# Optimization experiments

Hardware: AMD Instinct MI355X
Metric: run time of the kernel (lower is better)

The kernel has to match this reference:

```python
import jax, jax.numpy as jnp
import numpy as np

N_NODES = 100000


def gcn_conv(x, W, b, src, dst, n):
    """PyG GCNConv: add self-loops, symmetric degree norm, linear, scatter-add."""
    loop = jnp.arange(n, dtype=src.dtype)
    s = jnp.concatenate([src, loop])  # source nodes (message origin)
    d = jnp.concatenate([dst, loop])  # target nodes (aggregation)
    deg = jax.ops.segment_sum(jnp.ones_like(d, dtype=x.dtype), d, num_segments=n)
    dinv = jnp.where(deg > 0, jax.lax.rsqrt(deg), 0.0)
    norm = dinv[s] * dinv[d]  # [E+N]
    h = x @ W  # [N, out]
    msg = h[s] * norm[:, None]  # [E+N, out]
    return jax.ops.segment_sum(msg, d, num_segments=n) + b


def setup_inputs() -> dict:
    key = jax.random.key(0)
    ks = jax.random.split(key, 8)
    n, e, din, dh, dout = N_NODES, 3200000, 128, 64, 6
    x = jax.random.normal(ks[0], (n, din), dtype=jnp.float32)
    edge_index = jax.random.randint(ks[1], (2, e), 0, n, dtype=jnp.int64)
    sc = lambda f: 1.0 / np.sqrt(f)
    W1 = jax.random.normal(ks[2], (din, dh), dtype=jnp.float32) * sc(din)
    b1 = jnp.zeros((dh,), dtype=jnp.float32)
    W2 = jax.random.normal(ks[3], (dh, dh), dtype=jnp.float32) * sc(dh)
    b2 = jnp.zeros((dh,), dtype=jnp.float32)
    W3 = jax.random.normal(ks[4], (dh, dout), dtype=jnp.float32) * sc(dh)
    b3 = jnp.zeros((dout,), dtype=jnp.float32)
    return {"x": x, "edge_index": edge_index, "W1": W1, "b1": b1,
            "W2": W2, "b2": b2, "W3": W3, "b3": b3}


def reference(x, edge_index, W1, b1, W2, b2, W3, b3):
    n = x.shape[0]
    src, dst = edge_index[0], edge_index[1]
    # eval mode: dropout is identity
    h = jax.nn.relu(gcn_conv(x, W1, b1, src, dst, n))
    h = jax.nn.relu(gcn_conv(h, W2, b2, src, dst, n))
    h = gcn_conv(h, W3, b3, src, dst, n)
    return jax.nn.log_softmax(h, axis=1)
```

## Files before the change

kernel.cpp:

```cpp
#include <hip/hip_runtime.h>
#include <hip/hip_fp16.h>
#include <math.h>


#define WS_ALIGN(x) (((x) + 255) & ~(size_t)255)
#define BKN 256
#define CAP 9216
#define EPT 8
#define BIN_THR 512
#define BIN_CHUNK (BIN_THR * EPT)

typedef _Float16 half8 __attribute__((ext_vector_type(8)));
typedef float floatx4 __attribute__((ext_vector_type(4)));

__global__ __launch_bounds__(BIN_THR) void bin_kernel(
    const int* __restrict__ src, const int* __restrict__ dst,
    int* __restrict__ cur, int* __restrict__ slab, int E, int NB) {
    __shared__ int cnt[512];
    __shared__ int incl[512];
    __shared__ int gbase[512];
    __shared__ int stag[BIN_CHUNK];
    const int tid = threadIdx.x;
    const int base = blockIdx.x * BIN_CHUNK + tid * EPT;
    cnt[tid] = 0;
    __syncthreads();
    int b[EPT], w[EPT], lp[EPT];
    #pragma unroll
    for (int k = 0; k < EPT; ++k) {
        int e = base + k;
        if (e < E) {
            int s = src[e], d = dst[e];
            b[k] = d >> 8;
            w[k] = (s << 8) | (d & 255);
        } else b[k] = -1;
    }
    #pragma unroll
    for (int k = 0; k < EPT; ++k)
        if (b[k] >= 0) lp[k] = atomicAdd(&cnt[b[k]], 1);
    __syncthreads();
    incl[tid] = cnt[tid];
    __syncthreads();
    for (int off = 1; off < 512; off <<= 1) {
        int v = 0;
        if (tid >= off) v = incl[tid - off];
        __syncthreads();
        incl[tid] += v;
        __syncthreads();
    }
    if (tid < NB) {
        int c = cnt[tid];
        gbase[tid] = c ? atomicAdd(&cur[tid], c) : 0;
    }
    #pragma unroll
    for (int k = 0; k < EPT; ++k)
        if (b[k] >= 0) stag[incl[b[k]] - cnt[b[k]] + lp[k]] = w[k];
    __syncthreads();
    const int total = incl[NB - 1];
    for (int idx = tid; idx < total; idx += BIN_THR) {
        int wv = stag[idx];
        int lo = 0, hi = NB - 1;
        while (lo < hi) { int mid = (lo + hi) >> 1; if (incl[mid] > idx) hi = mid; else lo = mid + 1; }
        int excl = incl[lo] - cnt[lo];
        int p = gbase[lo] + (idx - excl);
        if (p < CAP) slab[(size_t)lo * CAP + p] = wv;
    }
}

__global__ __launch_bounds__(512) void bucket_sort_kernel(
    const int* __restrict__ slab, const int* __restrict__ cur,
    int* __restrict__ srcS, int2* __restrict__ rows,
    float* __restrict__ dinv, int n) {
    __shared__ int cnt[BKN], s[BKN], cursor[BKN];
    const int b = blockIdx.x, tid = threadIdx.x;
    const int m = min(cur[b], CAP);
    const int* sp = slab + (size_t)b * CAP;
    if (tid < BKN) cnt[tid] = 0;
    __syncthreads();
    for (int j = tid; j < m; j += 512) atomicAdd(&cnt[sp[j] & (BKN - 1)], 1);
    __syncthreads();
    if (tid < BKN) s[tid] = cnt[tid];
    __syncthreads();
    for (int off = 1; off < BKN; off <<= 1) {
        int v = 0;
        if (tid < BKN && tid >= off) v = s[tid - off];
        __syncthreads();
        if (tid < BKN) s[tid] += v;
        __syncthreads();
    }
    if (tid < BKN) {
        int ofs = s[tid] - cnt[tid];
        cursor[tid] = ofs;
        int node = b * BKN + tid;
        if (node < n) {
            rows[node] = make_int2(b * CAP + ofs, b * CAP + ofs + cnt[tid]);
            dinv[node] = rsqrtf((float)(cnt[tid] + 1));
        }
    }
    __syncthreads();
    for (int j = tid; j < m; j += 512) {
        int w = sp[j];
        int p = atomicAdd(&cursor[w & (BKN - 1)], 1);
        srcS[(size_t)b * CAP + p] = w >> 8;
    }
}

template <int K>
__global__ __launch_bounds__(256) void linear_mfma_f32_kernel(
    const float* __restrict__ Xf, const float* __restrict__ W,
    const float* __restrict__ dinv, _Float16* __restrict__ Y, int n) {
    constexpr int KC = K / 32;
    __shared__ _Float16 Bf[KC * 4 * 64 * 8];
    const int tid = threadIdx.x;
    for (int i = tid; i < KC * 4 * 64 * 8; i += 256) {
        int j = i & 7, lane = (i >> 3) & 63, tile = (i >> 9) & 3, kc = i >> 11;
        int k = kc * 32 + ((lane >> 4) << 3) + j;
        int col = tile * 16 + (lane & 15);
        Bf[i] = (_Float16)W[k * 64 + col];
    }
    __syncthreads();
    const int lane = tid & 63, wid = tid >> 6;
    const int mrow = lane & 15, quad = lane >> 4;
    #pragma unroll
    for (int tt = 0; tt < 4; ++tt) {
        const int base = (blockIdx.x * 4 + tt) * 64 + wid * 16;
        if (base >= n) continue;
        const int anode = min(base + mrow, n - 1);
        floatx4 acc[4] = {{0, 0, 0, 0}, {0, 0, 0, 0}, {0, 0, 0, 0}, {0, 0, 0, 0}};
        #pragma unroll
        for (int kc = 0; kc < KC; ++kc) {
            float4 xa = *(const float4*)&Xf[(size_t)anode * K + kc * 32 + quad * 8];
            float4 xb = *(const float4*)&Xf[(size_t)anode * K + kc * 32 + quad * 8 + 4];
            half8 a;
            a[0] = (_Float16)xa.x; a[1] = (_Float16)xa.y; a[2] = (_Float16)xa.z; a[3] = (_Float16)xa.w;
            a[4] = (_Float16)xb.x; a[5] = (_Float16)xb.y; a[6] = (_Float16)xb.z; a[7] = (_Float16)xb.w;
            #pragma unroll
            for (int t = 0; t < 4; ++t) {
                half8 b = *(const half8*)&Bf[((kc * 4 + t) * 64 + lane) * 8];
                acc[t] = __builtin_amdgcn_mfma_f32_16x16x32_f16(a, b, acc[t], 0, 0, 0);
            }
        }
        #pragma unroll
        for (int r = 0; r < 4; ++r) {
            int node = base + quad * 4 + r;
            if (node < n) {
                float di = dinv[node];
                #pragma unroll
                for (int t = 0; t < 4; ++t)
                    Y[(size_t)node * 64 + t * 16 + mrow] = (_Float16)(acc[t][r] * di);
            }
        }
    }
}

__global__ __launch_bounds__(256) void linear_mfma_f16_kernel(
    const _Float16* __restrict__ Xh, const float* __restrict__ W,
    const float* __restrict__ dinv, _Float16* __restrict__ Y, int n) {
    constexpr int K = 64, KC = 2;
    __shared__ _Float16 Bf[KC * 4 * 64 * 8];
    const int tid = threadIdx.x;
    for (int i = tid; i < KC * 4 * 64 * 8; i += 256) {
        int j = i & 7, lane = (i >> 3) & 63, tile = (i >> 9) & 3, kc = i >> 11;
        int k = kc * 32 + ((lane >> 4) << 3) + j;
        int col = tile * 16 + (lane & 15);
        Bf[i] = (_Float16)W[k * 64 + col];
    }
    __syncthreads();
    const int lane = tid & 63, wid = tid >> 6;
    const int mrow = lane & 15, quad = lane >> 4;
    #pragma unroll
    for (int tt = 0; tt < 4; ++tt) {
        const int base = (blockIdx.x * 4 + tt) * 64 + wid * 16;
        if (base >= n) continue;
        const int anode = min(base + mrow, n - 1);
        floatx4 acc[4] = {{0, 0, 0, 0}, {0, 0, 0, 0}, {0, 0, 0, 0}, {0, 0, 0, 0}};
        #pragma unroll
        for (int kc = 0; kc < KC; ++kc) {
            half8 a = *(const half8*)&Xh[(size_t)anode * K + kc * 32 + quad * 8];
            #pragma unroll
            for (int t = 0; t < 4; ++t) {
                half8 b = *(const half8*)&Bf[((kc * 4 + t) * 64 + lane) * 8];
                acc[t] = __builtin_amdgcn_mfma_f32_16x16x32_f16(a, b, acc[t], 0, 0, 0);
            }
        }
        #pragma unroll
        for (int r = 0; r < 4; ++r) {
            int node = base + quad * 4 + r;
            if (node < n) {
                float di = dinv[node];
                #pragma unroll
                for (int t = 0; t < 4; ++t)
                    Y[(size_t)node * 64 + t * 16 + mrow] = (_Float16)(acc[t][r] * di);
            }
        }
    }
}

__global__ __launch_bounds__(256) void linear3_kernel(const __half* __restrict__ Xh,
                                                      const float* __restrict__ W,
                                                      const float* __restrict__ dinv,
                                                      __half* __restrict__ Y, int n) {
    __shared__ float Wl[64 * 6];
    __shared__ float Xs[32][65];
    const int tid = threadIdx.x;
    for (int i = tid; i < 64 * 6; i += 256) Wl[i] = W[i];
    const int sub = tid >> 3;
    const int feat = tid & 7;
    for (int base = blockIdx.x * 32; base < n; base += gridDim.x * 32) {
        __syncthreads();
        for (int i = tid; i < 32 * 64; i += 256) {
            int r = i >> 6, c = i & 63;
            int node = base + r;
            Xs[r][c] = (node < n) ? __half2float(Xh[(size_t)node * 64 + c]) : 0.f;
        }
        __syncthreads();
        int node = base + sub;
        if (node < n) {
            float r = 0.f;
            if (feat < 6) {
                float acc = 0.f;
                #pragma unroll
                for (int k = 0; k < 64; ++k) acc = fmaf(Xs[sub][k], Wl[k * 6 + feat], acc);
                r = acc * dinv[node];
            }
            Y[(size_t)node * 8 + feat] = __float2half_rn(r);
        }
    }
}

__global__ __launch_bounds__(256) void agg64_kernel(
    const _Float16* __restrict__ Hs, const float* __restrict__ dinv,
    const int* __restrict__ srcS, const int2* __restrict__ rows,
    const float* __restrict__ bias, _Float16* __restrict__ Out,
    int n, int do_relu) {
    const int wave = (blockIdx.x * blockDim.x + threadIdx.x) >> 6;
    const int lane = threadIdx.x & 63;
    if (wave >= n) return;
    const int slot = lane >> 3;
    const int f8 = lane & 7;
    const int2 row = rows[wave];
    const int beg = row.x, end = row.y;
    half8 hA, hB;
    #pragma unroll
    for (int i = 0; i < 8; ++i) { hA[i] = (_Float16)0.f; hB[i] = (_Float16)0.f; }
    int j = beg;
    for (; j + 32 <= end; j += 32) {
        int s0 = srcS[j      + slot];
        int s1 = srcS[j + 8  + slot];
        int s2 = srcS[j + 16 + slot];
        int s3 = srcS[j + 24 + slot];
        half8 v0 = *(const half8*)&Hs[(size_t)s0 * 64 + f8 * 8];
        half8 v1 = *(const half8*)&Hs[(size_t)s1 * 64 + f8 * 8];
        half8 v2 = *(const half8*)&Hs[(size_t)s2 * 64 + f8 * 8];
        half8 v3 = *(const half8*)&Hs[(size_t)s3 * 64 + f8 * 8];
        hA += v0; hB += v1; hA += v2; hB += v3;
    }
    for (; j + 16 <= end; j += 16) {
        int s0 = srcS[j + slot];
        int s1 = srcS[j + 8 + slot];
        half8 v0 = *(const half8*)&Hs[(size_t)s0 * 64 + f8 * 8];
        half8 v1 = *(const half8*)&Hs[(size_t)s1 * 64 + f8 * 8];
        hA += v0; hB += v1;
    }
    for (; j < end; j += 8) {
        int jj = j + slot;
        if (jj < end) {
            half8 v = *(const half8*)&Hs[(size_t)srcS[jj] * 64 + f8 * 8];
            hA += v;
        }
    }
    half8 ht = hA + hB;
    #pragma unroll
    for (int mask = 8; mask <= 32; mask <<= 1) {
        int4 ci = *(int4*)&ht, oi;
        oi.x = __shfl_xor(ci.x, mask);
        oi.y = __shfl_xor(ci.y, mask);
        oi.z = __shfl_xor(ci.z, mask);
        oi.w = __shfl_xor(ci.w, mask);
        ht += *(half8*)&oi;
    }
    half8 self = *(const half8*)&Hs[(size_t)wave * 64 + f8 * 8];
    const float di = dinv[wave];
    float4 b0 = *(const float4*)&bias[f8 * 8];
    float4 b1 = *(const float4*)&bias[f8 * 8 + 4];
    float bb[8] = {b0.x, b0.y, b0.z, b0.w, b1.x, b1.y, b1.z, b1.w};
    half8 o;
    #pragma unroll
    for (int i = 0; i < 8; ++i) {
        float t = ((float)ht[i] + (float)self[i]) * di + bb[i];
        if (do_relu) t = fmaxf(t, 0.f);
        o[i] = (_Float16)t;
    }
    if (slot == 0) *(half8*)&Out[(size_t)wave * 64 + f8 * 8] = o;
}

__global__ __launch_bounds__(256) void agg6_lsm_kernel(
    const _Float16* __restrict__ Hs6, const float* __restrict__ dinv,
    const int* __restrict__ srcS, const int2* __restrict__ rows,
    const float* __restrict__ bias, float* __restrict__ out, int n) {
    const int wave = (blockIdx.x * blockDim.x + threadIdx.x) >> 6;
    const int lane = threadIdx.x & 63;
    if (wave >= n) return;
    const int2 row = rows[wave];
    const int beg = row.x, end = row.y;
    half8 ht;
    #pragma unroll
    for (int i = 0; i < 8; ++i) ht[i] = (_Float16)0.f;
    for (int j = beg + lane; j < end; j += 64) {
        int s = srcS[j];
        ht += *(const half8*)&Hs6[(size_t)s * 8];
    }
    #pragma unroll
    for (int mask = 1; mask <= 32; mask <<= 1) {
        int4 ci = *(int4*)&ht, oi;
        oi.x = __shfl_xor(ci.x, mask);
        oi.y = __shfl_xor(ci.y, mask);
        oi.z = __shfl_xor(ci.z, mask);
        oi.w = __shfl_xor(ci.w, mask);
        ht += *(half8*)&oi;
    }
    half8 self = *(const half8*)&Hs6[(size_t)wave * 8];
    const float di = dinv[wave];
    float a[6];
    #pragma unroll
    for (int q = 0; q < 6; ++q)
        a[q] = ((float)ht[q] + (float)self[q]) * di + bias[q];
    float mx = a[0];
    #pragma unroll
    for (int q = 1; q < 6; ++q) mx = fmaxf(mx, a[q]);
    float sum = 0.f;
    #pragma unroll
    for (int q = 0; q < 6; ++q) sum += expf(a[q] - mx);
    float lse = mx + logf(sum);
    if (lane == 0) {
        float* op = &out[(size_t)wave * 6];
        *(float2*)(op)     = make_float2(a[0] - lse, a[1] - lse);
        *(float2*)(op + 2) = make_float2(a[2] - lse, a[3] - lse);
        *(float2*)(op + 4) = make_float2(a[4] - lse, a[5] - lse);
    }
}

extern "C" void kernel_launch(void* const* d_in, const int* in_sizes, int n_in,
                              void* d_out, int out_size, void* d_ws, size_t ws_size,
                              hipStream_t stream) {
    const float* x  = (const float*)d_in[0];
    const int*   ei = (const int*)d_in[1];
    const float* W1 = (const float*)d_in[2];
    const float* b1 = (const float*)d_in[3];
    const float* W2 = (const float*)d_in[4];
    const float* b2 = (const float*)d_in[5];
    const float* W3 = (const float*)d_in[6];
    const float* b3 = (const float*)d_in[7];
    float* out = (float*)d_out;

    const int n = in_sizes[0] / 128;
    const int E = in_sizes[1] / 2;
    const int* src = ei;
    const int* dst = ei + E;
    const int NB = (n + BKN - 1) / BKN;

    char* ws = (char*)d_ws;
    auto carve = [&](size_t bytes) { char* p = ws; ws += WS_ALIGN(bytes); return p; };
    int*      cur  = (int*)     carve((size_t)NB * 4);
    float*    dinv = (float*)   carve((size_t)n * 4);
    int*      slab = (int*)     carve((size_t)NB * CAP * 4);
    int*      srcS = (int*)     carve((size_t)NB * CAP * 4);
    int2*     rows = (int2*)    carve((size_t)n * 8);
    _Float16* hsA  = (_Float16*)carve((size_t)n * 64 * 2 + 4096);
    _Float16* hsB  = (_Float16*)carve((size_t)n * 64 * 2 + 4096);
    _Float16* hsC  = (_Float16*)carve((size_t)n * 8 * 2);
    (void)ws_size; (void)n_in; (void)out_size;

    (void)hipMemsetAsync(cur, 0, (size_t)NB * 4, stream);
    bin_kernel<<<(E + BIN_CHUNK - 1) / BIN_CHUNK, BIN_THR, 0, stream>>>(src, dst, cur, slab, E, NB);
    bucket_sort_kernel<<<NB, 512, 0, stream>>>(slab, cur, srcS, rows, dinv, n);

    const int aggGrid = (n + 3) / 4;
    const int linGrid = (n + 255) / 256;

    linear_mfma_f32_kernel<128><<<linGrid, 256, 0, stream>>>(x, W1, dinv, hsA, n);
    agg64_kernel<<<aggGrid, 256, 0, stream>>>(hsA, dinv, srcS, rows, b1, hsB, n, 1);

    linear_mfma_f16_kernel<<<linGrid, 256, 0, stream>>>(hsB, W2, dinv, hsA, n);
    agg64_kernel<<<aggGrid, 256, 0, stream>>>(hsA, dinv, srcS, rows, b2, hsB, n, 1);

    linear3_kernel<<<2048, 256, 0, stream>>>((const __half*)hsB, W3, dinv, (__half*)hsC, n);
    agg6_lsm_kernel<<<(n + 3) / 4, 256, 0, stream>>>(hsC, dinv, srcS, rows, b3, out, n);
}
```

Measured before the change: 356.0 us.

## Aggregate before transform in layer 2 and fuse layer-2/3 linears into aggregation

```diff
diff --git a/kernel.cpp b/kernel.cpp
--- a/kernel.cpp
+++ b/kernel.cpp
@@ -11,6 +11,7 @@
 #define BIN_CHUNK (BIN_THR * EPT)
 
 typedef _Float16 half8 __attribute__((ext_vector_type(8)));
+typedef _Float16 half2v __attribute__((ext_vector_type(2)));
 typedef float floatx4 __attribute__((ext_vector_type(4)));
 
 __global__ __launch_bounds__(BIN_THR) void bin_kernel(
@@ -121,8 +122,8 @@
     const int lane = tid & 63, wid = tid >> 6;
     const int mrow = lane & 15, quad = lane >> 4;
     #pragma unroll
-    for (int tt = 0; tt < 4; ++tt) {
-        const int base = (blockIdx.x * 4 + tt) * 64 + wid * 16;
+    for (int tt = 0; tt < 2; ++tt) {
+        const int base = (blockIdx.x * 2 + tt) * 64 + wid * 16;
         if (base >= n) continue;
         const int anode = min(base + mrow, n - 1);
         floatx4 acc[4] = {{0, 0, 0, 0}, {0, 0, 0, 0}, {0, 0, 0, 0}, {0, 0, 0, 0}};
@@ -152,86 +153,11 @@
     }
 }
 
-__global__ __launch_bounds__(256) void linear_mfma_f16_kernel(
-    const _Float16* __restrict__ Xh, const float* __restrict__ W,
-    const float* __restrict__ dinv, _Float16* __restrict__ Y, int n) {
-    constexpr int K = 64, KC = 2;
-    __shared__ _Float16 Bf[KC * 4 * 64 * 8];
-    const int tid = threadIdx.x;
-    for (int i = tid; i < KC * 4 * 64 * 8; i += 256) {
-        int j = i & 7, lane = (i >> 3) & 63, tile = (i >> 9) & 3, kc = i >> 11;
-        int k = kc * 32 + ((lane >> 4) << 3) + j;
-        int col = tile * 16 + (lane & 15);
-        Bf[i] = (_Float16)W[k * 64 + col];
-    }
-    __syncthreads();
-    const int lane = tid & 63, wid = tid >> 6;
-    const int mrow = lane & 15, quad = lane >> 4;
-    #pragma unroll
-    for (int tt = 0; tt < 4; ++tt) {
-        const int base = (blockIdx.x * 4 + tt) * 64 + wid * 16;
-        if (base >= n) continue;
-        const int anode = min(base + mrow, n - 1);
-        floatx4 acc[4] = {{0, 0, 0, 0}, {0, 0, 0, 0}, {0, 0, 0, 0}, {0, 0, 0, 0}};
-        #pragma unroll
-        for (int kc = 0; kc < KC; ++kc) {
-            half8 a = *(const half8*)&Xh[(size_t)anode * K + kc * 32 + quad * 8];
-            #pragma unroll
-            for (int t = 0; t < 4; ++t) {
-                half8 b = *(const half8*)&Bf[((kc * 4 + t) * 64 + lane) * 8];
-                acc[t] = __builtin_amdgcn_mfma_f32_16x16x32_f16(a, b, acc[t], 0, 0, 0);
-            }
-        }
-        #pragma unroll
-        for (int r = 0; r < 4; ++r) {
-            int node = base + quad * 4 + r;
-            if (node < n) {
-                float di = dinv[node];
-                #pragma unroll
-                for (int t = 0; t < 4; ++t)
-                    Y[(size_t)node * 64 + t * 16 + mrow] = (_Float16)(acc[t][r] * di);
-            }
-        }
-    }
-}
-
-__global__ __launch_bounds__(256) void linear3_kernel(const __half* __restrict__ Xh,
-                                                      const float* __restrict__ W,
-                                                      const float* __restrict__ dinv,
-                                                      __half* __restrict__ Y, int n) {
-    __shared__ float Wl[64 * 6];
-    __shared__ float Xs[32][65];
-    const int tid = threadIdx.x;
-    for (int i = tid; i < 64 * 6; i += 256) Wl[i] = W[i];
-    const int sub = tid >> 3;
-    const int feat = tid & 7;
-    for (int base = blockIdx.x * 32; base < n; base += gridDim.x * 32) {
-        __syncthreads();
-        for (int i = tid; i < 32 * 64; i += 256) {
-            int r = i >> 6, c = i & 63;
-            int node = base + r;
-            Xs[r][c] = (node < n) ? __half2float(Xh[(size_t)node * 64 + c]) : 0.f;
-        }
-        __syncthreads();
-        int node = base + sub;
-        if (node < n) {
-            float r = 0.f;
-            if (feat < 6) {
-                float acc = 0.f;
-                #pragma unroll
-                for (int k = 0; k < 64; ++k) acc = fmaf(Xs[sub][k], Wl[k * 6 + feat], acc);
-                r = acc * dinv[node];
-            }
-            Y[(size_t)node * 8 + feat] = __float2half_rn(r);
-        }
-    }
-}
-
 __global__ __launch_bounds__(256) void agg64_kernel(
     const _Float16* __restrict__ Hs, const float* __restrict__ dinv,
     const int* __restrict__ srcS, const int2* __restrict__ rows,
     const float* __restrict__ bias, _Float16* __restrict__ Out,
-    int n, int do_relu) {
+    int n, int do_relu, int post_scale) {
     const int wave = (blockIdx.x * blockDim.x + threadIdx.x) >> 6;
     const int lane = threadIdx.x & 63;
     if (wave >= n) return;
@@ -288,9 +214,115 @@
     for (int i = 0; i < 8; ++i) {
         float t = ((float)ht[i] + (float)self[i]) * di + bb[i];
         if (do_relu) t = fmaxf(t, 0.f);
+        if (post_scale) t *= di;
         o[i] = (_Float16)t;
     }
     if (slot == 0) *(half8*)&Out[(size_t)wave * 64 + f8 * 8] = o;
+}
+
+__global__ __launch_bounds__(256) void aggB_kernel(
+    const _Float16* __restrict__ H1s, const float* __restrict__ dinv,
+    const int* __restrict__ srcS, const int2* __restrict__ rows,
+    const float* __restrict__ W2, const float* __restrict__ b2,
+    const float* __restrict__ W3, __half* __restrict__ Yc, int n) {
+    __shared__ half2v W2p[32 * 64];
+    __shared__ float  W3l[64 * 6];
+    __shared__ _Float16 uL[4][64];
+    const int tid = threadIdx.x;
+    for (int i = tid; i < 32 * 64; i += 256) {
+        int t = i >> 6, o = i & 63;
+        half2v v;
+        v[0] = (_Float16)W2[(2 * t) * 64 + o];
+        v[1] = (_Float16)W2[(2 * t + 1) * 64 + o];
+        W2p[i] = v;
+    }
+    for (int i = tid; i < 64 * 6; i += 256) W3l[i] = W3[i];
+    __syncthreads();
+    const int wid = tid >> 6, lane = tid & 63;
+    const int wave = blockIdx.x * 4 + wid;
+    if (wave >= n) return;
+    const int slot = lane >> 3;
+    const int f8 = lane & 7;
+    const int2 row = rows[wave];
+    const int beg = row.x, end = row.y;
+    half8 hA, hB;
+    #pragma unroll
+    for (int i = 0; i < 8; ++i) { hA[i] = (_Float16)0.f; hB[i] = (_Float16)0.f; }
+    int j = beg;
+    for (; j + 32 <= end; j += 32) {
+        int s0 = srcS[j      + slot];
+        int s1 = srcS[j + 8  + slot];
+        int s2 = srcS[j + 16 + slot];
+        int s3 = srcS[j + 24 + slot];
+        half8 v0 = *(const half8*)&H1s[(size_t)s0 * 64 + f8 * 8];
+        half8 v1 = *(const half8*)&H1s[(size_t)s1 * 64 + f8 * 8];
+        half8 v2 = *(const half8*)&H1s[(size_t)s2 * 64 + f8 * 8];
+        half8 v3 = *(const half8*)&H1s[(size_t)s3 * 64 + f8 * 8];
+        hA += v0; hB += v1; hA += v2; hB += v3;
+    }
+    for (; j + 16 <= end; j += 16) {
+        int s0 = srcS[j + slot];
+        int s1 = srcS[j + 8 + slot];
+        half8 v0 = *(const half8*)&H1s[(size_t)s0 * 64 + f8 * 8];
+        half8 v1 = *(const half8*)&H1s[(size_t)s1 * 64 + f8 * 8];
+        hA += v0; hB += v1;
+    }
+    for (; j < end; j += 8) {
+        int jj = j + slot;
+        if (jj < end) {
+            half8 v = *(const half8*)&H1s[(size_t)srcS[jj] * 64 + f8 * 8];
+            hA += v;
+        }
+    }
+    half8 ht = hA + hB;
+    #pragma unroll
+    for (int mask = 8; mask <= 32; mask <<= 1) {
+        int4 ci = *(int4*)&ht, oi;
+        oi.x = __shfl_xor(ci.x, mask);
+        oi.y = __shfl_xor(ci.y, mask);
+        oi.z = __shfl_xor(ci.z, mask);
+        oi.w = __shfl_xor(ci.w, mask);
+        ht += *(half8*)&oi;
+    }
+    half8 self = *(const half8*)&H1s[(size_t)wave * 64 + f8 * 8];
+    const float di = dinv[wave];
+    half8 u;
+    #pragma unroll
+    for (int i = 0; i < 8; ++i)
+        u[i] = (_Float16)(((float)ht[i] + (float)self[i]) * di);
+    if (slot == 0) *(half8*)&uL[wid][f8 * 8] = u;
+    float acc = b2[lane];
+    const half2v* up = (const half2v*)&uL[wid][0];
+    #pragma unroll
+    for (int t = 0; t < 32; ++t) {
+        half2v uv = up[t];
+        half2v wv = W2p[t * 64 + lane];
+#if defined(__has_builtin)
+#if __has_builtin(__builtin_amdgcn_fdot2)
+        acc = __builtin_amdgcn_fdot2(uv, wv, acc, false);
+#else
+        acc += (float)uv[0] * (float)wv[0] + (float)uv[1] * (float)wv[1];
+#endif
+#else
+        acc += (float)uv[0] * (float)wv[0] + (float)uv[1] * (float)wv[1];
+#endif
+    }
+    float h2 = fmaxf(acc, 0.f);
+    float p[6];
+    #pragma unroll
+    for (int q = 0; q < 6; ++q) p[q] = h2 * W3l[lane * 6 + q];
+    #pragma unroll
+    for (int mask = 1; mask <= 32; mask <<= 1) {
+        #pragma unroll
+        for (int q = 0; q < 6; ++q) p[q] += __shfl_xor(p[q], mask);
+    }
+    if (lane == 0) {
+        half8 o;
+        #pragma unroll
+        for (int q = 0; q < 6; ++q) o[q] = (_Float16)(p[q] * di);
+        o[6] = (_Float16)0.f; o[7] = (_Float16)0.f;
+        *(half8*)&Yc[(size_t)wave * 8] = o;
+    }
 }
 
 __global__ __launch_bounds__(256) void agg6_lsm_kernel(
@@ -375,14 +407,12 @@
     bucket_sort_kernel<<<NB, 512, 0, stream>>>(slab, cur, srcS, rows, dinv, n);
 
     const int aggGrid = (n + 3) / 4;
-    const int linGrid = (n + 255) / 256;
+    const int linGrid = (n + 127) / 128;
 
     linear_mfma_f32_kernel<128><<<linGrid, 256, 0, stream>>>(x, W1, dinv, hsA, n);
-    agg64_kernel<<<aggGrid, 256, 0, stream>>>(hsA, dinv, srcS, rows, b1, hsB, n, 1);
-
-    linear_mfma_f16_kernel<<<linGrid, 256, 0, stream>>>(hsB, W2, dinv, hsA, n);
-    agg64_kernel<<<aggGrid, 256, 0, stream>>>(hsA, dinv, srcS, rows, b2, hsB, n, 1);
-
-    linear3_kernel<<<2048, 256, 0, stream>>>((const __half*)hsB, W3, dinv, (__half*)hsC, n);
-    agg6_lsm_kernel<<<(n + 3) / 4, 256, 0, stream>>>(hsC, dinv, srcS, rows, b3, out, n);
-}
+    agg64_kernel<<<aggGrid, 256, 0, stream>>>(hsA, dinv, srcS, rows, b1, hsB, n, 1, 1);
+
+    aggB_kernel<<<aggGrid, 256, 0, stream>>>(hsB, dinv, srcS, rows, W2, b2, W3, (__half*)hsC, n);
+
+    agg6_lsm_kernel<<<aggGrid, 256, 0, stream>>>(hsC, dinv, srcS, rows, b3, out, n);
+}
```

Result: slower. 379.6 us (+6.6%).

## Fuse edge binning with layer-1 linear and fold layer-3 linear into aggregation

Applied to the files above, without the earlier changes.

```diff
diff --git a/kernel.cpp b/kernel.cpp
--- a/kernel.cpp
+++ b/kernel.cpp
@@ -13,56 +13,103 @@
 typedef _Float16 half8 __attribute__((ext_vector_type(8)));
 typedef float floatx4 __attribute__((ext_vector_type(4)));
 
-__global__ __launch_bounds__(BIN_THR) void bin_kernel(
+__global__ __launch_bounds__(512) void fat_bin_lin1_kernel(
     const int* __restrict__ src, const int* __restrict__ dst,
-    int* __restrict__ cur, int* __restrict__ slab, int E, int NB) {
-    __shared__ int cnt[512];
-    __shared__ int incl[512];
-    __shared__ int gbase[512];
-    __shared__ int stag[BIN_CHUNK];
+    int* __restrict__ cur, int* __restrict__ slab, int E, int NB, int binG,
+    const float* __restrict__ Xf, const float* __restrict__ W1,
+    _Float16* __restrict__ Y, int n) {
+    __shared__ int smem[5632];
     const int tid = threadIdx.x;
-    const int base = blockIdx.x * BIN_CHUNK + tid * EPT;
-    cnt[tid] = 0;
-    __syncthreads();
-    int b[EPT], w[EPT], lp[EPT];
-    #pragma unroll
-    for (int k = 0; k < EPT; ++k) {
-        int e = base + k;
-        if (e < E) {
-            int s = src[e], d = dst[e];
-            b[k] = d >> 8;
-            w[k] = (s << 8) | (d & 255);
-        } else b[k] = -1;
-    }
-    #pragma unroll
-    for (int k = 0; k < EPT; ++k)
-        if (b[k] >= 0) lp[k] = atomicAdd(&cnt[b[k]], 1);
-    __syncthreads();
-    incl[tid] = cnt[tid];
-    __syncthreads();
-    for (int off = 1; off < 512; off <<= 1) {
-        int v = 0;
-        if (tid >= off) v = incl[tid - off];
-        __syncthreads();
-        incl[tid] += v;
-        __syncthreads();
-    }
-    if (tid < NB) {
-        int c = cnt[tid];
-        gbase[tid] = c ? atomicAdd(&cur[tid], c) : 0;
-    }
-    #pragma unroll
-    for (int k = 0; k < EPT; ++k)
-        if (b[k] >= 0) stag[incl[b[k]] - cnt[b[k]] + lp[k]] = w[k];
-    __syncthreads();
-    const int total = incl[NB - 1];
-    for (int idx = tid; idx < total; idx += BIN_THR) {
-        int wv = stag[idx];
-        int lo = 0, hi = NB - 1;
-        while (lo < hi) { int mid = (lo + hi) >> 1; if (incl[mid] > idx) hi = mid; else lo = mid + 1; }
-        int excl = incl[lo] - cnt[lo];
-        int p = gbase[lo] + (idx - excl);
-        if (p < CAP) slab[(size_t)lo * CAP + p] = wv;
+    if (blockIdx.x < binG) {
+        int* cnt   = smem;
+        int* incl  = smem + 512;
+        int* gbase = smem + 1024;
+        int* stag  = smem + 1536;
+        const int base = blockIdx.x * BIN_CHUNK + tid * EPT;
+        cnt[tid] = 0;
+        __syncthreads();
+        int b[EPT], w[EPT], lp[EPT];
+        #pragma unroll
+        for (int k = 0; k < EPT; ++k) {
+            int e = base + k;
+            if (e < E) {
+                int s = src[e], d = dst[e];
+                b[k] = d >> 8;
+                w[k] = (s << 8) | (d & 255);
+            } else b[k] = -1;
+        }
+        #pragma unroll
+        for (int k = 0; k < EPT; ++k)
+            if (b[k] >= 0) lp[k] = atomicAdd(&cnt[b[k]], 1);
+        __syncthreads();
+        incl[tid] = cnt[tid];
+        __syncthreads();
+        for (int off = 1; off < 512; off <<= 1) {
+            int v = 0;
+            if (tid >= off) v = incl[tid - off];
+            __syncthreads();
+            incl[tid] += v;
+            __syncthreads();
+        }
+        if (tid < NB) {
+            int c = cnt[tid];
+            gbase[tid] = c ? atomicAdd(&cur[tid], c) : 0;
+        }
+        #pragma unroll
+        for (int k = 0; k < EPT; ++k)
+            if (b[k] >= 0) stag[incl[b[k]] - cnt[b[k]] + lp[k]] = w[k];
+        __syncthreads();
+        const int total = incl[NB - 1];
+        for (int idx = tid; idx < total; idx += BIN_THR) {
+            int wv = stag[idx];
+            int lo = 0, hi = NB - 1;
+            while (lo < hi) { int mid = (lo + hi) >> 1; if (incl[mid] > idx) hi = mid; else lo = mid + 1; }
+            int excl = incl[lo] - cnt[lo];
+            int p = gbase[lo] + (idx - excl);
+            if (p < CAP) slab[(size_t)lo * CAP + p] = wv;
+        }
+    } else {
+        constexpr int K = 128, KC = 4;
+        _Float16* Bf = (_Float16*)smem;
+        for (int i = tid; i < KC * 4 * 64 * 8; i += 512) {
+            int j = i & 7, lane = (i >> 3) & 63, tile = (i >> 9) & 3, kc = i >> 11;
+            int k = kc * 32 + ((lane >> 4) << 3) + j;
+            int col = tile * 16 + (lane & 15);
+            Bf[i] = (_Float16)W1[k * 64 + col];
+        }
+        __syncthreads();
+        const int lane = tid & 63, wid = tid >> 6;
+        const int mrow = lane & 15, quad = lane >> 4;
+        const int lblk = blockIdx.x - binG;
+        #pragma unroll
+        for (int tt = 0; tt < 2; ++tt) {
+            const int base = lblk * 256 + wid * 32 + tt * 16;
+            if (base >= n) continue;
+            const int anode = min(base + mrow, n - 1);
+            floatx4 acc[4] = {{0, 0, 0, 0}, {0, 0, 0, 0}, {0, 0, 0, 0}, {0, 0, 0, 0}};
+            #pragma unroll
+            for (int kc = 0; kc < KC; ++kc) {
+                float4 xa = *(const float4*)&Xf[(size_t)anode * K + kc * 32 + quad * 8];
+                float4 xb = *(const float4*)&Xf[(size_t)anode * K + kc * 32 + quad * 8 + 4];
+                half8 a;
+                a[0] = (_Float16)xa.x; a[1] = (_Float16)xa.y; a[2] = (_Float16)xa.z; a[3] = (_Float16)xa.w;
+                a[4] = (_Float16)xb.x; a[5] = (_Float16)xb.y; a[6] = (_Float16)xb.z; a[7] = (_Float16)xb.w;
+                #pragma unroll
+                for (int t = 0; t < 4; ++t) {
+                    half8 b = *(const half8*)&Bf[((kc * 4 + t) * 64 + lane) * 8];
+                    acc[t] = __builtin_amdgcn_mfma_f32_16x16x32_f16(a, b, acc[t], 0, 0, 0);
+                }
+            }
+            #pragma unroll
+            for (int r = 0; r < 4; ++r) {
+                int node = base + quad * 4 + r;
+                if (node < n) {
+                    #pragma unroll
+                    for (int t = 0; t < 4; ++t)
+                        Y[(size_t)node * 64 + t * 16 + mrow] = (_Float16)acc[t][r];
+                }
+            }
+        }
     }
 }
 
@@ -101,54 +148,6 @@
         int w = sp[j];
         int p = atomicAdd(&cursor[w & (BKN - 1)], 1);
         srcS[(size_t)b * CAP + p] = w >> 8;
-    }
-}
-
-template <int K>
-__global__ __launch_bounds__(256) void linear_mfma_f32_kernel(
-    const float* __restrict__ Xf, const float* __restrict__ W,
-    const float* __restrict__ dinv, _Float16* __restrict__ Y, int n) {
-    constexpr int KC = K / 32;
-    __shared__ _Float16 Bf[KC * 4 * 64 * 8];
-    const int tid = threadIdx.x;
-    for (int i = tid; i < KC * 4 * 64 * 8; i += 256) {
-        int j = i & 7, lane = (i >> 3) & 63, tile = (i >> 9) & 3, kc = i >> 11;
-        int k = kc * 32 + ((lane >> 4) << 3) + j;
-        int col = tile * 16 + (lane & 15);
-        Bf[i] = (_Float16)W[k * 64 + col];
-    }
-    __syncthreads();
-    const int lane = tid & 63, wid = tid >> 6;
-    const int mrow = lane & 15, quad = lane >> 4;
-    #pragma unroll
-    for (int tt = 0; tt < 4; ++tt) {
-        const int base = (blockIdx.x * 4 + tt) * 64 + wid * 16;
-        if (base >= n) continue;
-        const int anode = min(base + mrow, n - 1);
-        floatx4 acc[4] = {{0, 0, 0, 0}, {0, 0, 0, 0}, {0, 0, 0, 0}, {0, 0, 0, 0}};
-        #pragma unroll
-        for (int kc = 0; kc < KC; ++kc) {
-            float4 xa = *(const float4*)&Xf[(size_t)anode * K + kc * 32 + quad * 8];
-            float4 xb = *(const float4*)&Xf[(size_t)anode * K + kc * 32 + quad * 8 + 4];
-            half8 a;
-            a[0] = (_Float16)xa.x; a[1] = (_Float16)xa.y; a[2] = (_Float16)xa.z; a[3] = (_Float16)xa.w;
-            a[4] = (_Float16)xb.x; a[5] = (_Float16)xb.y; a[6] = (_Float16)xb.z; a[7] = (_Float16)xb.w;
-            #pragma unroll
-            for (int t = 0; t < 4; ++t) {
-                half8 b = *(const half8*)&Bf[((kc * 4 + t) * 64 + lane) * 8];
-                acc[t] = __builtin_amdgcn_mfma_f32_16x16x32_f16(a, b, acc[t], 0, 0, 0);
-            }
-        }
-        #pragma unroll
-        for (int r = 0; r < 4; ++r) {
-            int node = base + quad * 4 + r;
-            if (node < n) {
-                float di = dinv[node];
-                #pragma unroll
-                for (int t = 0; t < 4; ++t)
-                    Y[(size_t)node * 64 + t * 16 + mrow] = (_Float16)(acc[t][r] * di);
-            }
-        }
     }
 }
 
@@ -195,45 +194,89 @@
     }
 }
 
-__global__ __launch_bounds__(256) void linear3_kernel(const __half* __restrict__ Xh,
-                                                      const float* __restrict__ W,
-                                                      const float* __restrict__ dinv,
-                                                      __half* __restrict__ Y, int n) {
-    __shared__ float Wl[64 * 6];
-    __shared__ float Xs[32][65];
-    const int tid = threadIdx.x;
-    for (int i = tid; i < 64 * 6; i += 256) Wl[i] = W[i];
-    const int sub = tid >> 3;
-    const int feat = tid & 7;
-    for (int base = blockIdx.x * 32; base < n; base += gridDim.x * 32) {
-        __syncthreads();
-        for (int i = tid; i < 32 * 64; i += 256) {
-            int r = i >> 6, c = i & 63;
-            int node = base + r;
-            Xs[r][c] = (node < n) ? __half2float(Xh[(size_t)node * 64 + c]) : 0.f;
-        }
-        __syncthreads();
-        int node = base + sub;
-        if (node < n) {
-            float r = 0.f;
-            if (feat < 6) {
-                float acc = 0.f;
-                #pragma unroll
-                for (int k = 0; k < 64; ++k) acc = fmaf(Xs[sub][k], Wl[k * 6 + feat], acc);
-                r = acc * dinv[node];
-            }
-            Y[(size_t)node * 8 + feat] = __float2half_rn(r);
-        }
-    }
-}
-
-__global__ __launch_bounds__(256) void agg64_kernel(
+__global__ __launch_bounds__(256) void agg64s_kernel(
+    const _Float16* __restrict__ H1, const float* __restrict__ dinv,
+    const int* __restrict__ srcS, const int2* __restrict__ rows,
+    const float* __restrict__ bias, _Float16* __restrict__ Out, int n) {
+    const int wave = (blockIdx.x * blockDim.x + threadIdx.x) >> 6;
+    const int lane = threadIdx.x & 63;
+    if (wave >= n) return;
+    const int slot = lane >> 3;
+    const int f8 = lane & 7;
+    const int2 row = rows[wave];
+    const int beg = row.x, end = row.y;
+    half8 hA, hB;
+    #pragma unroll
+    for (int i = 0; i < 8; ++i) { hA[i] = (_Float16)0.f; hB[i] = (_Float16)0.f; }
+    int j = beg;
+    for (; j + 32 <= end; j += 32) {
+        int s0 = srcS[j      + slot];
+        int s1 = srcS[j + 8  + slot];
+        int s2 = srcS[j + 16 + slot];
+        int s3 = srcS[j + 24 + slot];
+        _Float16 d0 = (_Float16)dinv[s0];
+        _Float16 d1 = (_Float16)dinv[s1];
+        _Float16 d2 = (_Float16)dinv[s2];
+        _Float16 d3 = (_Float16)dinv[s3];
+        half8 v0 = *(const half8*)&H1[(size_t)s0 * 64 + f8 * 8];
+        half8 v1 = *(const half8*)&H1[(size_t)s1 * 64 + f8 * 8];
+        half8 v2 = *(const half8*)&H1[(size_t)s2 * 64 + f8 * 8];
+        half8 v3 = *(const half8*)&H1[(size_t)s3 * 64 + f8 * 8];
+        hA += v0 * d0; hB += v1 * d1; hA += v2 * d2; hB += v3 * d3;
+    }
+    for (; j + 16 <= end; j += 16) {
+        int s0 = srcS[j + slot];
+        int s1 = srcS[j + 8 + slot];
+        _Float16 d0 = (_Float16)dinv[s0];
+        _Float16 d1 = (_Float16)dinv[s1];
+        half8 v0 = *(const half8*)&H1[(size_t)s0 * 64 + f8 * 8];
+        half8 v1 = *(const half8*)&H1[(size_t)s1 * 64 + f8 * 8];
+        hA += v0 * d0; hB += v1 * d1;
+    }
+    for (; j < end; j += 8) {
+        int jj = j + slot;
+        if (jj < end) {
+            int s0 = srcS[jj];
+            _Float16 d0 = (_Float16)dinv[s0];
+            half8 v = *(const half8*)&H1[(size_t)s0 * 64 + f8 * 8];
+            hA += v * d0;
+        }
+    }
+    half8 ht = hA + hB;
+    #pragma unroll
+    for (int mask = 8; mask <= 32; mask <<= 1) {
+        int4 ci = *(int4*)&ht, oi;
+        oi.x = __shfl_xor(ci.x, mask);
+        oi.y = __shfl_xor(ci.y, mask);
+        oi.z = __shfl_xor(ci.z, mask);
+        oi.w = __shfl_xor(ci.w, mask);
+        ht += *(half8*)&oi;
+    }
+    half8 self = *(const half8*)&H1[(size_t)wave * 64 + f8 * 8];
+    const float di = dinv[wave];
+    float4 b0 = *(const float4*)&bias[f8 * 8];
+    float4 b1v = *(const float4*)&bias[f8 * 8 + 4];
+    float bb[8] = {b0.x, b0.y, b0.z, b0.w, b1v.x, b1v.y, b1v.z, b1v.w};
+    half8 o;
+    #pragma unroll
+    for (int i = 0; i < 8; ++i) {
+        float t = ((float)ht[i] + di * (float)self[i]) * di + bb[i];
+        o[i] = (_Float16)fmaxf(t, 0.f);
+    }
+    if (slot == 0) *(half8*)&Out[(size_t)wave * 64 + f8 * 8] = o;
+}
+
+__global__ __launch_bounds__(256) void agg64w3_kernel(
     const _Float16* __restrict__ Hs, const float* __restrict__ dinv,
     const int* __restrict__ srcS, const int2* __restrict__ rows,
-    const float* __restrict__ bias, _Float16* __restrict__ Out,
-    int n, int do_relu) {
-    const int wave = (blockIdx.x * blockDim.x + threadIdx.x) >> 6;
-    const int lane = threadIdx.x & 63;
+    const float* __restrict__ bias, const float* __restrict__ W3,
+    __half* __restrict__ Yc, int n) {
+    __shared__ float W3l[64 * 6];
+    const int tid = threadIdx.x;
+    for (int i = tid; i < 64 * 6; i += 256) W3l[i] = W3[i];
+    __syncthreads();
+    const int wave = (blockIdx.x * blockDim.x + tid) >> 6;
+    const int lane = tid & 63;
     if (wave >= n) return;
     const int slot = lane >> 3;
     const int f8 = lane & 7;
@@ -281,16 +324,28 @@
     half8 self = *(const half8*)&Hs[(size_t)wave * 64 + f8 * 8];
     const float di = dinv[wave];
     float4 b0 = *(const float4*)&bias[f8 * 8];
-    float4 b1 = *(const float4*)&bias[f8 * 8 + 4];
-    float bb[8] = {b0.x, b0.y, b0.z, b0.w, b1.x, b1.y, b1.z, b1.w};
-    half8 o;
+    float4 b1v = *(const float4*)&bias[f8 * 8 + 4];
+    float bb[8] = {b0.x, b0.y, b0.z, b0.w, b1v.x, b1v.y, b1v.z, b1v.w};
+    float p[6] = {0.f, 0.f, 0.f, 0.f, 0.f, 0.f};
     #pragma unroll
     for (int i = 0; i < 8; ++i) {
-        float t = ((float)ht[i] + (float)self[i]) * di + bb[i];
-        if (do_relu) t = fmaxf(t, 0.f);
-        o[i] = (_Float16)t;
-    }
-    if (slot == 0) *(half8*)&Out[(size_t)wave * 64 + f8 * 8] = o;
+        float h2 = fmaxf(((float)ht[i] + (float)self[i]) * di + bb[i], 0.f);
+        const float* wr = &W3l[(f8 * 8 + i) * 6];
+        #pragma unroll
+        for (int q = 0; q < 6; ++q) p[q] = fmaf(h2, wr[q], p[q]);
+    }
+    #pragma unroll
+    for (int mask = 1; mask <= 4; mask <<= 1) {
+        #pragma unroll
+        for (int q = 0; q < 6; ++q) p[q] += __shfl_xor(p[q], mask);
+    }
+    if (lane == 0) {
+        half8 o;
+        #pragma unroll
+        for (int q = 0; q < 6; ++q) o[q] = (_Float16)(p[q] * di);
+        o[6] = (_Float16)0.f; o[7] = (_Float16)0.f;
+        *(half8*)&Yc[(size_t)wave * 8] = o;
+    }
 }
 
 __global__ __launch_bounds__(256) void agg6_lsm_kernel(
@@ -370,19 +425,21 @@
     _Float16* hsC  = (_Float16*)carve((size_t)n * 8 * 2);
     (void)ws_size; (void)n_in; (void)out_size;
 
+    const int binG = (E + BIN_CHUNK - 1) / BIN_CHUNK;
+    const int linG = (n + 255) / 256;
+    const int aggGrid = (n + 3) / 4;
+
     (void)hipMemsetAsync(cur, 0, (size_t)NB * 4, stream);
-    bin_kernel<<<(E + BIN_CHUNK - 1) / BIN_CHUNK, BIN_THR, 0, stream>>>(src, dst, cur, slab, E, NB);
+    fat_bin_lin1_kernel<<<binG + linG, 512, 0, stream>>>(
+        src, dst, cur, slab, E, NB, binG, x, W1, hsA, n);
+
     bucket_sort_kernel<<<NB, 512, 0, stream>>>(slab, cur, srcS, rows, dinv, n);
 
-    const int aggGrid = (n + 3) / 4;
-    const int linGrid = (n + 255) / 256;
-
-    linear_mfma_f32_kernel<128><<<linGrid, 256, 0, stream>>>(x, W1, dinv, hsA, n);
-    agg64_kernel<<<aggGrid, 256, 0, stream>>>(hsA, dinv, srcS, rows, b1, hsB, n, 1);
-
-    linear_mfma_f16_kernel<<<linGrid, 256, 0, stream>>>(hsB, W2, dinv, hsA, n);
-    agg64_kernel<<<aggGrid, 256, 0, stream>>>(hsA, dinv, srcS, rows, b2, hsB, n, 1);
-
-    linear3_kernel<<<2048, 256, 0, stream>>>((const __half*)hsB, W3, dinv, (__half*)hsC, n);
-    agg6_lsm_kernel<<<(n + 3) / 4, 256, 0, stream>>>(hsC, dinv, srcS, rows, b3, out, n);
-}
+    agg64s_kernel<<<aggGrid, 256, 0, stream>>>(hsA, dinv, srcS, rows, b1, hsB, n);
+
+    linear_mfma_f16_kernel<<<(n + 255) / 256, 256, 0, stream>>>(hsB, W2, dinv, hsA, n);
+
+    agg64w3_kernel<<<aggGrid, 256, 0, stream>>>(hsA, dinv, srcS, rows, b2, W3, (__half*)hsC, n);
+
+    agg6_lsm_kernel<<<aggGrid, 256, 0, stream>>>(hsC, dinv, srcS, rows, b3, out, n);
+}
```

After: 344.5 us. 1.03x faster.
